# Kernel tuning notes

Hardware: AMD Instinct MI355X
Metric: run time of the kernel (lower is better)

The kernel has to match this reference:

```python
import jax, jax.numpy as jnp
import numpy as np

NUM_ITERS = 3

def squash(t):
    # t: [..., D]; squash along last axis exactly as the torch code:
    # sn * t / ((1+sn) * sqrt(sn))
    sn = jnp.sum(t * t, axis=-1, keepdims=True)
    return sn * t / ((1.0 + sn) * jnp.sqrt(sn))

def setup_inputs() -> dict:
    key = jax.random.key(0)
    k_x, k_w = jax.random.split(key)
    B, O, I, D_out, D_in = 512, 10, 1152, 16, 8
    x = jax.random.normal(k_x, (B, I, D_in), dtype=jnp.float32)
    W = 0.01 * jax.random.normal(k_w, (O, I, D_out, D_in), dtype=jnp.float32)
    return {"x": x, "W": W}

def reference(x, W):
    B = x.shape[0]
    O, I, D_out, _ = W.shape
    # x_hat[b,o,i,d] = sum_e W[o,i,d,e] * x[b,i,e]
    x_hat = jnp.einsum('oide,bie->boid', W, x)          # [B,O,I,D_out]
    x_hat_det = jax.lax.stop_gradient(x_hat)
    b = jnp.zeros((B, O, I), dtype=x.dtype)
    for it in range(NUM_ITERS):
        c = jax.nn.softmax(b, axis=1)                   # over out caps
        if it == NUM_ITERS - 1:
            outputs = squash(jnp.sum(c[:, :, :, None] * x_hat, axis=-2, keepdims=True))
        else:
            outputs = squash(jnp.sum(c[:, :, :, None] * x_hat_det, axis=-2, keepdims=True))
            b = b + jnp.sum(outputs * x_hat_det, axis=-1)
    outputs = jnp.squeeze(outputs, axis=-2)             # [B,O,D_out]
    # decode_idx == -1 branch: pick longest capsule
    classes = jax.nn.softmax(jnp.sqrt(jnp.sum(outputs ** 2, axis=2)), axis=1)  # [B,O]
    idx = jnp.argmax(classes, axis=1)                   # [B]
    masked = jnp.eye(O, dtype=outputs.dtype)[idx]       # [B,O]
    t = jnp.sum(outputs * masked[:, :, None], axis=1)[:, None, :]  # [B,1,D_out]
    return (t, outputs)
```

## Files before the change

kernel.cpp:

```cpp
#include <hip/hip_runtime.h>

#define BB 512
#define OO 10
#define II 1152
#define DD 16
#define EE 8
#define GB 32
#define IC 64
#define ILEN (II / IC)
#define NBLK ((BB / GB) * IC)
#define XROW (ILEN * 2 + 1)
#define WSLAB (II * DD * EE / 4)

typedef float v2f __attribute__((ext_vector_type(2)));
typedef float v4f __attribute__((ext_vector_type(4)));

__device__ __forceinline__ v2f pk_mul(v2f a, v2f b) {
    v2f d;
    asm("v_pk_mul_f32 %0, %1, %2" : "=v"(d) : "v"(a), "v"(b));
    return d;
}
__device__ __forceinline__ v2f pk_fma(v2f a, v2f b, v2f c) {
    v2f d;
    asm("v_pk_fma_f32 %0, %1, %2, %3" : "=v"(d) : "v"(a), "v"(b), "v"(c));
    return d;
}

__device__ __forceinline__ float dot8(v4f wa, v4f wb, v4f xa, v4f xb) {
    v2f p = pk_mul(wa.lo, xa.lo);
    p = pk_fma(wa.hi, xa.hi, p);
    p = pk_fma(wb.lo, xb.lo, p);
    p = pk_fma(wb.hi, xb.hi, p);
    return p.x + p.y;
}

template <int CTRL>
__device__ __forceinline__ float dpp_add(float v) {
    int s = __builtin_amdgcn_update_dpp(0, __float_as_int(v), CTRL, 0xf, 0xf, true);
    return v + __int_as_float(s);
}
__device__ __forceinline__ float dred16(float v) {
    v = dpp_add<0xB1>(v);
    v = dpp_add<0x4E>(v);
    v = dpp_add<0x141>(v);
    v = dpp_add<0x140>(v);
    return v;
}

__device__ __forceinline__ float squash_lane(float sv) {
    float sn = dred16(sv * sv);
    return sv * (sn / ((1.0f + sn) * sqrtf(sn)));
}

template <int PASS>
__global__ __launch_bounds__(256, 4)
void caps_pass(const float* __restrict__ x, const float* __restrict__ W,
               float* __restrict__ s_out,
               const float* __restrict__ s0, const float* __restrict__ s1) {
    __shared__ v4f xlds[GB * XROW];

    const int tid = threadIdx.x;
    const int d = tid & 15;
    const int g = tid >> 4;
    const int bg = blockIdx.x >> 6;
    const int ic = blockIdx.x & 63;
    const int b0 = bg * GB + g;
    const int b1 = b0 + 16;
    const int i0 = ic * ILEN;

    const v4f* x4 = (const v4f*)x;
    for (int k = tid; k < GB * ILEN * 2; k += 256) {
        const int gg = k / (ILEN * 2);
        const int rem = k - gg * (ILEN * 2);
        xlds[gg * XROW + rem] =
            x4[(size_t)(bg * GB + gg) * (II * EE / 4) + (size_t)i0 * 2 + rem];
    }

    constexpr float LOG2E = 1.44269504f;
    float vr0[OO], vr1[OO];
    if constexpr (PASS >= 1) {
        #pragma unroll
        for (int o = 0; o < OO; o++) {
            float v = squash_lane(s0[(b0 * OO + o) * DD + d]);
            float w = squash_lane(s0[(b1 * OO + o) * DD + d]);
            if constexpr (PASS == 2) {
                v += squash_lane(s1[(b0 * OO + o) * DD + d]);
                w += squash_lane(s1[(b1 * OO + o) * DD + d]);
            }
            vr0[o] = v * LOG2E;
            vr1[o] = w * LOG2E;
        }
    }
    __syncthreads();

    float sa0[OO], sa1[OO];
    #pragma unroll
    for (int o = 0; o < OO; o++) { sa0[o] = 0.0f; sa1[o] = 0.0f; }

    const v4f* W4 = (const v4f*)W;
    int widx = (i0 * DD + d) * 2;

    for (int ii = 0; ii < ILEN; ii++) {
        const v4f xa0 = xlds[g * XROW + ii * 2 + 0];
        const v4f xb0 = xlds[g * XROW + ii * 2 + 1];
        const v4f xa1 = xlds[(g + 16) * XROW + ii * 2 + 0];
        const v4f xb1 = xlds[(g + 16) * XROW + ii * 2 + 1];

        float xh0[OO], xh1[OO];
        #pragma unroll
        for (int o = 0; o < OO; o++) {
            const v4f wa = W4[o * WSLAB + widx];
            const v4f wb = W4[o * WSLAB + widx + 1];
            xh0[o] = dot8(wa, wb, xa0, xb0);
            xh1[o] = dot8(wa, wb, xa1, xb1);
        }

        if constexpr (PASS == 0) {
            #pragma unroll
            for (int o = 0; o < OO; o++) { sa0[o] += xh0[o]; sa1[o] += xh1[o]; }
        } else {
            float e0[OO], e1[OO];
            float se0 = 0.0f, se1 = 0.0f;
            #pragma unroll
            for (int o = 0; o < OO; o++) {
                e0[o] = __builtin_amdgcn_exp2f(dred16(vr0[o] * xh0[o]));
                e1[o] = __builtin_amdgcn_exp2f(dred16(vr1[o] * xh1[o]));
                se0 += e0[o];
                se1 += e1[o];
            }
            const float inv0 = __builtin_amdgcn_rcpf(se0);
            const float inv1 = __builtin_amdgcn_rcpf(se1);
            #pragma unroll
            for (int o = 0; o < OO; o++) {
                sa0[o] = fmaf(e0[o] * inv0, xh0[o], sa0[o]);
                sa1[o] = fmaf(e1[o] * inv1, xh1[o], sa1[o]);
            }
        }
        widx += DD * 2;
    }

    const float scale = (PASS == 0) ? 0.1f : 1.0f;
    #pragma unroll
    for (int o = 0; o < OO; o++) {
        atomicAdd(&s_out[(b0 * OO + o) * DD + d], sa0[o] * scale);
        atomicAdd(&s_out[(b1 * OO + o) * DD + d], sa1[o] * scale);
    }
}

__global__ __launch_bounds__(192)
void caps_final(const float* __restrict__ s2, float* __restrict__ out) {
    __shared__ float norml[12];
    const int b = blockIdx.x;
    const int tid = threadIdx.x;
    const int d = tid & 15;
    const int o = tid >> 4;

    float v = 0.0f;
    if (o < OO) {
        const float sv = s2[(b * OO + o) * DD + d];
        const float sn = dred16(sv * sv);
        v = sv * (sn / ((1.0f + sn) * sqrtf(sn)));
        out[BB * DD + (b * OO + o) * DD + d] = v;
        if (d == 0) norml[o] = sn;
    }
    __syncthreads();

    int idx = 0;
    float best = norml[0];
    #pragma unroll
    for (int oo = 1; oo < OO; oo++) {
        const float n = norml[oo];
        if (n > best) { best = n; idx = oo; }
    }
    if (o == idx) out[b * DD + d] = v;
}

extern "C" void kernel_launch(void* const* d_in, const int* in_sizes, int n_in,
                              void* d_out, int out_size, void* d_ws, size_t ws_size,
                              hipStream_t stream) {
    const float* x = (const float*)d_in[0];
    const float* W = (const float*)d_in[1];
    float* out = (float*)d_out;

    float* s0 = (float*)d_ws;
    float* s1 = s0 + BB * OO * DD;
    float* s2 = s1 + BB * OO * DD;

    hipMemsetAsync(d_ws, 0, (size_t)3 * BB * OO * DD * sizeof(float), stream);

    caps_pass<0><<<NBLK, 256, 0, stream>>>(x, W, s0, nullptr, nullptr);
    caps_pass<1><<<NBLK, 256, 0, stream>>>(x, W, s1, s0, nullptr);
    caps_pass<2><<<NBLK, 256, 0, stream>>>(x, W, s2, s0, s1);
    caps_final<<<BB, 192, 0, stream>>>(s2, out);
}
```

Baseline: 248.2 us.

## Replace atomic accumulation with per-chunk partial buffers and separate reduction kernels

Each pass now writes its per-chunk partial sums to a dedicated slice of a large workspace buffer (128 chunks) instead of issuing float atomicAdds into a shared accumulator. Separate reduce kernels sum the partials, and the final kernel folds in the last reduction. The change also doubles the number of input chunks and raises the occupancy hint to 8 waves. This removes atomic contention and the memset, but adds roughly 42 MB of partial-buffer traffic per pass and two extra launches. It falls back to the atomic path when the workspace is too small.

```diff
diff --git a/kernel.cpp b/kernel.cpp
--- a/kernel.cpp
+++ b/kernel.cpp
@@ -6,10 +6,7 @@
 #define DD 16
 #define EE 8
 #define GB 32
-#define IC 64
-#define ILEN (II / IC)
-#define NBLK ((BB / GB) * IC)
-#define XROW (ILEN * 2 + 1)
+#define BOD (BB * OO * DD)
 #define WSLAB (II * DD * EE / 4)
 
 typedef float v2f __attribute__((ext_vector_type(2)));
@@ -52,18 +49,20 @@
     return sv * (sn / ((1.0f + sn) * sqrtf(sn)));
 }
 
-template <int PASS>
-__global__ __launch_bounds__(256, 4)
+template <int PASS, int IC, int MINW, bool ATOMIC>
+__global__ __launch_bounds__(256, MINW)
 void caps_pass(const float* __restrict__ x, const float* __restrict__ W,
                float* __restrict__ s_out,
                const float* __restrict__ s0, const float* __restrict__ s1) {
+    constexpr int ILEN = II / IC;
+    constexpr int XROW = ILEN * 2 + 1;
     __shared__ v4f xlds[GB * XROW];
 
     const int tid = threadIdx.x;
     const int d = tid & 15;
     const int g = tid >> 4;
-    const int bg = blockIdx.x >> 6;
-    const int ic = blockIdx.x & 63;
+    const int bg = blockIdx.x / IC;
+    const int ic = blockIdx.x & (IC - 1);
     const int b0 = bg * GB + g;
     const int b1 = b0 + 16;
     const int i0 = ic * ILEN;
@@ -139,16 +138,36 @@
         widx += DD * 2;
     }
 
-    const float scale = (PASS == 0) ? 0.1f : 1.0f;
-    #pragma unroll
-    for (int o = 0; o < OO; o++) {
-        atomicAdd(&s_out[(b0 * OO + o) * DD + d], sa0[o] * scale);
-        atomicAdd(&s_out[(b1 * OO + o) * DD + d], sa1[o] * scale);
-    }
-}
-
+    if constexpr (ATOMIC) {
+        const float scale = (PASS == 0) ? 0.1f : 1.0f;
+        #pragma unroll
+        for (int o = 0; o < OO; o++) {
+            atomicAdd(&s_out[(b0 * OO + o) * DD + d], sa0[o] * scale);
+            atomicAdd(&s_out[(b1 * OO + o) * DD + d], sa1[o] * scale);
+        }
+    } else {
+        float* P = s_out + (size_t)ic * BOD;
+        #pragma unroll
+        for (int o = 0; o < OO; o++) {
+            P[(b0 * OO + o) * DD + d] = sa0[o];
+            P[(b1 * OO + o) * DD + d] = sa1[o];
+        }
+    }
+}
+
+template <int IC>
+__global__ __launch_bounds__(256)
+void caps_reduce(const float* __restrict__ P, float* __restrict__ s, float scale) {
+    const int idx = blockIdx.x * 256 + threadIdx.x;
+    float a = 0.0f;
+    #pragma unroll 8
+    for (int ic = 0; ic < IC; ic++) a += P[(size_t)ic * BOD + idx];
+    s[idx] = a * scale;
+}
+
+template <int IC, bool FUSED>
 __global__ __launch_bounds__(192)
-void caps_final(const float* __restrict__ s2, float* __restrict__ out) {
+void caps_final(const float* __restrict__ src, float* __restrict__ out) {
     __shared__ float norml[12];
     const int b = blockIdx.x;
     const int tid = threadIdx.x;
@@ -157,10 +176,18 @@
 
     float v = 0.0f;
     if (o < OO) {
-        const float sv = s2[(b * OO + o) * DD + d];
+        float sv;
+        const int idx = (b * OO + o) * DD + d;
+        if constexpr (FUSED) {
+            sv = 0.0f;
+            #pragma unroll 8
+            for (int ic = 0; ic < IC; ic++) sv += src[(size_t)ic * BOD + idx];
+        } else {
+            sv = src[idx];
+        }
         const float sn = dred16(sv * sv);
         v = sv * (sn / ((1.0f + sn) * sqrtf(sn)));
-        out[BB * DD + (b * OO + o) * DD + d] = v;
+        out[BB * DD + idx] = v;
         if (d == 0) norml[o] = sn;
     }
     __syncthreads();
@@ -182,14 +209,32 @@
     const float* W = (const float*)d_in[1];
     float* out = (float*)d_out;
 
-    float* s0 = (float*)d_ws;
-    float* s1 = s0 + BB * OO * DD;
-    float* s2 = s1 + BB * OO * DD;
-
-    hipMemsetAsync(d_ws, 0, (size_t)3 * BB * OO * DD * sizeof(float), stream);
-
-    caps_pass<0><<<NBLK, 256, 0, stream>>>(x, W, s0, nullptr, nullptr);
-    caps_pass<1><<<NBLK, 256, 0, stream>>>(x, W, s1, s0, nullptr);
-    caps_pass<2><<<NBLK, 256, 0, stream>>>(x, W, s2, s0, s1);
-    caps_final<<<BB, 192, 0, stream>>>(s2, out);
-}
+    constexpr int ICP = 128;
+    const size_t needP = ((size_t)ICP * BOD + 2 * BOD) * sizeof(float);
+
+    if (ws_size >= needP) {
+        float* P  = (float*)d_ws;
+        float* s0 = P + (size_t)ICP * BOD;
+        float* s1 = s0 + BOD;
+        constexpr int NB = (BB / GB) * ICP;
+
+        caps_pass<0, ICP, 8, false><<<NB, 256, 0, stream>>>(x, W, P, nullptr, nullptr);
+        caps_reduce<ICP><<<BOD / 256, 256, 0, stream>>>(P, s0, 0.1f);
+        caps_pass<1, ICP, 8, false><<<NB, 256, 0, stream>>>(x, W, P, s0, nullptr);
+        caps_reduce<ICP><<<BOD / 256, 256, 0, stream>>>(P, s1, 1.0f);
+        caps_pass<2, ICP, 8, false><<<NB, 256, 0, stream>>>(x, W, P, s0, s1);
+        caps_final<ICP, true><<<BB, 192, 0, stream>>>(P, out);
+    } else {
+        constexpr int ICA = 64;
+        float* s0 = (float*)d_ws;
+        float* s1 = s0 + BOD;
+        float* s2 = s1 + BOD;
+        constexpr int NB = (BB / GB) * ICA;
+
+        hipMemsetAsync(d_ws, 0, (size_t)3 * BOD * sizeof(float), stream);
+        caps_pass<0, ICA, 4, true><<<NB, 256, 0, stream>>>(x, W, s0, nullptr, nullptr);
+        caps_pass<1, ICA, 4, true><<<NB, 256, 0, stream>>>(x, W, s1, s0, nullptr);
+        caps_pass<2, ICA, 4, true><<<NB, 256, 0, stream>>>(x, W, s2, s0, s1);
+        caps_final<1, false><<<BB, 192, 0, stream>>>(s2, out);
+    }
+}
```

New measurement: 518.8 us. 2.09x slower.
